# Kernel optimization log

Measured on AMD Instinct MI355X. Metric: run time of the kernel, lower is better.

Reference implementation:

```python
import jax, jax.numpy as jnp
import numpy as np
from jax import lax

SIM_THRESH = 0.9
MOTION_SCALE = 0.5
SALIENCY_SCALE = 0.5
EPS = 1e-6


def setup_inputs() -> dict:
    key = jax.random.key(0)
    k1, k2, k3, k4 = jax.random.split(key, 4)
    B, N, D, H, W = 128, 196, 768, 14, 14
    return {
        "tokens": jax.random.normal(k1, (B, N, D), dtype=jnp.float32),
        "motion_magnitude": jax.random.uniform(k2, (B, 1, H, W), dtype=jnp.float32),
        "saliency_map": jax.random.uniform(k3, (B, 1, H, W), dtype=jnp.float32),
        "compression_ratio": jax.random.uniform(k4, (B, H, W), dtype=jnp.float32),
    }


def _importance(motion, saliency, ratio):
    # motion/saliency are already (B,1,14,14) == (height,width), so
    # adaptive_avg_pool2d to (14,14) is the identity.
    B = motion.shape[0]
    m = motion.reshape(B, -1)
    m = m / (jnp.max(m) + EPS)               # global max, as in torch .max()
    s = saliency.reshape(B, -1)
    s = s / (jnp.max(s) + EPS)
    r = ratio.reshape(B, -1)
    imp = (MOTION_SCALE * m + SALIENCY_SCALE * s
           + (1.0 - MOTION_SCALE - SALIENCY_SCALE) * r)
    lo = imp.min(axis=1, keepdims=True)
    hi = imp.max(axis=1, keepdims=True)
    return (imp - lo) / (hi - lo + EPS)      # (B, N)


def _groups(adj):
    """Sequential BFS grouping over roots, faithful to the torch loop.

    adj: bool (N,N) directed edge mask. Returns (group_ids int32 (N,), num_groups).
    """
    N = adj.shape[0]

    def root_step(carry, r):
        assigned, gids, gid = carry

        def assign(c):
            assigned, gids, gid = c
            # BFS from root r, only through currently-unassigned nodes
            allowed = (~assigned).at[r].set(True)
            reach0 = jnp.zeros(N, dtype=bool).at[r].set(True)

            def body(s):
                reach, _ = s
                nxt = reach | (jnp.any(adj & reach[:, None], axis=0) & allowed)
                return nxt, jnp.any(nxt != reach)

            reach, _ = lax.while_loop(lambda s: s[1], body, (reach0, True))
            return assigned | reach, jnp.where(reach, gid, gids), gid + 1

        carry = lax.cond(assigned[r], lambda c: c, assign, carry)
        return carry, None

    init = (jnp.zeros(N, dtype=bool), jnp.zeros(N, dtype=jnp.int32), jnp.int32(0))
    (_, gids, ngroups), _ = lax.scan(root_step, init, jnp.arange(N))
    return gids, ngroups


def _merge_one(tokens_b, imp_b, adj_b):
    N = tokens_b.shape[0]
    gids, ng = _groups(adj_b)
    denom = jax.ops.segment_sum(imp_b, gids, num_segments=N) + EPS
    w = imp_b / denom[gids]
    merged = jax.ops.segment_sum(tokens_b * w[:, None], gids, num_segments=N)
    return merged, gids, ng


def reference(tokens, motion_magnitude, saliency_map, compression_ratio):
    B, N, D = tokens.shape
    imp = _importance(motion_magnitude, saliency_map, compression_ratio)  # (B,N)

    # cosine similarity (F.normalize with eps=1e-12)
    norm = jnp.maximum(jnp.linalg.norm(tokens, axis=-1, keepdims=True), 1e-12)
    tn = tokens / norm
    sim = jnp.einsum('bnd,bmd->bnm', tn, tn)
    sim = sim * (1.0 - jnp.eye(N, dtype=sim.dtype))  # zero diagonal

    # directed merge mask: similarity * (1 - importance_row)
    mask = (sim > SIM_THRESH).astype(sim.dtype) * (1.0 - imp[:, :, None])
    adj = mask > 0.5

    merged, gids, ng = jax.vmap(_merge_one)(tokens, imp, adj)
    # merged padded to N groups (rows >= num_groups are zero)
    return merged, sim, imp, gids
```

## Files before the change

### kernel.cpp

```cpp
#include <hip/hip_runtime.h>
#include <cstdint>

static constexpr int cB = 128;
static constexpr int cN = 196;
static constexpr int cD = 768;
static constexpr int cNN = cN * cN;
static constexpr int cND = cN * cD;
static constexpr float cEPS = 1e-6f;
static constexpr size_t cBND = (size_t)cB * cN * cD;

typedef __attribute__((ext_vector_type(8))) short short8;
typedef __attribute__((ext_vector_type(4))) float f32x4;
typedef unsigned long long u64;

__device__ __forceinline__ unsigned short bf16_rne(float x) {
    unsigned u = __builtin_bit_cast(unsigned, x);
    u += 0x7FFFu + ((u >> 16) & 1u);
    return (unsigned short)(u >> 16);
}

__global__ __launch_bounds__(256) void k_imp(const float* __restrict__ mo,
                                             const float* __restrict__ sa,
                                             float* __restrict__ out_imp,
                                             float* __restrict__ ws_imp,
                                             float* __restrict__ ws_w,
                                             u64* __restrict__ ws_adj) {
    int b = blockIdx.x, t = threadIdx.x;
    __shared__ float redm[4], reds[4], lo_s[4], hi_s[4], MS[2], LOHI[2];

    for (int i = b * 256 + t; i < cB * cN * 4; i += cB * 256) ws_adj[i] = 0ull;

    float mm = 0.f, ms = 0.f;
    for (int i = t; i < cB * cN; i += 256) {
        mm = fmaxf(mm, mo[i]);
        ms = fmaxf(ms, sa[i]);
    }
    #pragma unroll
    for (int off = 32; off; off >>= 1) {
        mm = fmaxf(mm, __shfl_down(mm, off));
        ms = fmaxf(ms, __shfl_down(ms, off));
    }
    if ((t & 63) == 0) { redm[t >> 6] = mm; reds[t >> 6] = ms; }
    __syncthreads();
    if (t == 0) {
        float a = redm[0], c = reds[0];
        for (int w = 1; w < 4; w++) { a = fmaxf(a, redm[w]); c = fmaxf(c, reds[w]); }
        MS[0] = 1.0f / (a + cEPS);
        MS[1] = 1.0f / (c + cEPS);
    }
    __syncthreads();
    float Minv = MS[0], Sinv = MS[1];
    float v = 0.f, lo = 1e30f, hi = -1e30f;
    if (t < cN) {
        v = 0.5f * mo[b * cN + t] * Minv + 0.5f * sa[b * cN + t] * Sinv;
        lo = v; hi = v;
    }
    #pragma unroll
    for (int off = 32; off; off >>= 1) {
        lo = fminf(lo, __shfl_down(lo, off));
        hi = fmaxf(hi, __shfl_down(hi, off));
    }
    if ((t & 63) == 0) { lo_s[t >> 6] = lo; hi_s[t >> 6] = hi; }
    __syncthreads();
    if (t == 0) {
        float l = lo_s[0], h = hi_s[0];
        for (int w = 1; w < 4; w++) { l = fminf(l, lo_s[w]); h = fmaxf(h, hi_s[w]); }
        LOHI[0] = l; LOHI[1] = h;
    }
    __syncthreads();
    if (t < cN) {
        float imp = (v - LOHI[0]) / (LOHI[1] - LOHI[0] + cEPS);
        out_imp[b * cN + t] = imp;
        ws_imp[b * cN + t] = imp;
        ws_w[b * cN + t] = imp / (imp + cEPS);
    }
}

__global__ __launch_bounds__(256) void k_prep(const float* __restrict__ tok,
                                              const float* __restrict__ ws_w,
                                              unsigned short* __restrict__ plane,
                                              float* __restrict__ ws_invn,
                                              float* __restrict__ merged,
                                              int write_merged) {
    int wid = blockIdx.x * 4 + (threadIdx.x >> 6);
    int lane = threadIdx.x & 63;
    if (wid >= cB * cN) return;
    const float4* p4 = (const float4*)(tok + (size_t)wid * cD);
    float4 v[3];
    float s = 0.f;
    #pragma unroll
    for (int r = 0; r < 3; r++) {
        v[r] = p4[lane + 64 * r];
        s += v[r].x * v[r].x + v[r].y * v[r].y + v[r].z * v[r].z + v[r].w * v[r].w;
    }
    #pragma unroll
    for (int off = 32; off; off >>= 1) s += __shfl_xor(s, off);
    if (lane == 0) ws_invn[wid] = 1.0f / fmaxf(sqrtf(s), 1e-12f);
    float w = ws_w[wid];
    ushort4* hp = (ushort4*)(plane + (size_t)wid * cD);
    float4* mp = (float4*)(merged + (size_t)wid * cD);
    #pragma unroll
    for (int r = 0; r < 3; r++) {
        ushort4 h;
        h.x = bf16_rne(v[r].x);
        h.y = bf16_rne(v[r].y);
        h.z = bf16_rne(v[r].z);
        h.w = bf16_rne(v[r].w);
        hp[lane + 64 * r] = h;
        if (write_merged) {
            float4 m = v[r];
            m.x *= w; m.y *= w; m.z *= w; m.w *= w;
            mp[lane + 64 * r] = m;
        }
    }
}

__global__ __launch_bounds__(256, 2) void k_sim(const unsigned short* __restrict__ plane,
                                                const float* __restrict__ ws_invn,
                                                const float* __restrict__ ws_imp,
                                                float* __restrict__ out_sim,
                                                u64* __restrict__ ws_adj) {
    __shared__ unsigned short sA[128 * 40];
    __shared__ unsigned short sB[128 * 40];
    __shared__ float invR[128], invC[128], impR[128];
    __shared__ u64 ldsAdj[256];

    int bid = blockIdx.x;
    int xcd = bid & 7;
    int lin = bid >> 3;
    int b   = xcd + 8 * (lin >> 2);
    int tile = lin & 3;
    int rb = (tile >> 1) * 128, cb = (tile & 1) * 128;

    int t = threadIdx.x;
    int w = t >> 6, lane = t & 63;
    int lr = lane & 15, kf = (lane >> 4) * 8;
    int wr = (w >> 1) * 64, wc = (w & 1) * 64;

    const size_t bN = (size_t)b * cN;

    ldsAdj[t] = 0ull;
    if (t < 128) {
        int gr = rb + t;
        invR[t] = (gr < cN) ? ws_invn[bN + gr] : 0.f;
        impR[t] = (gr < cN) ? ws_imp[bN + gr] : 1.f;
    } else {
        int gc = cb + (t - 128);
        invC[t - 128] = (gc < cN) ? ws_invn[bN + gc] : 0.f;
    }

    f32x4 acc[4][4];
    #pragma unroll
    for (int i = 0; i < 4; i++)
        #pragma unroll
        for (int j = 0; j < 4; j++) acc[i][j] = (f32x4){0.f, 0.f, 0.f, 0.f};

    int srow = t >> 2;
    int q = t & 3;

    for (int k0 = 0; k0 < cD; k0 += 32) {
        #pragma unroll
        for (int p = 0; p < 2; ++p) {
            int row = srow + 64 * p;
            size_t koff = (size_t)k0 + 8 * q;
            uint4 va = make_uint4(0u, 0u, 0u, 0u), vb = va;
            int gr = rb + row;
            if (gr < cN) va = *(const uint4*)(plane + (bN + gr) * cD + koff);
            int gc = cb + row;
            if (gc < cN) vb = *(const uint4*)(plane + (bN + gc) * cD + koff);
            *(uint4*)&sA[row * 40 + 8 * q] = va;
            *(uint4*)&sB[row * 40 + 8 * q] = vb;
        }
        __syncthreads();

        short8 af[4], bf[4];
        #pragma unroll
        for (int rg = 0; rg < 4; rg++)
            af[rg] = *(const short8*)&sA[(wr + 16 * rg + lr) * 40 + kf];
        #pragma unroll
        for (int cg = 0; cg < 4; cg++)
            bf[cg] = *(const short8*)&sB[(wc + 16 * cg + lr) * 40 + kf];
        #pragma unroll
        for (int rg = 0; rg < 4; rg++)
            #pragma unroll
            for (int cg = 0; cg < 4; cg++)
                acc[rg][cg] = __builtin_amdgcn_mfma_f32_16x16x32_bf16(af[rg], bf[cg], acc[rg][cg], 0, 0, 0);
        __syncthreads();
    }

    float* so = out_sim + (size_t)b * cNN;
    int wloc = w >> 1;
    #pragma unroll
    for (int rg = 0; rg < 4; rg++) {
        int rBaseLoc = wr + 16 * rg + (lane >> 4) * 4;
        #pragma unroll
        for (int cg = 0; cg < 4; cg++) {
            int cLoc = wc + 16 * cg + lr;
            int C = cb + cLoc;
            if (C >= cN) continue;
            float ic = invC[cLoc];
            u64 bits = 0ull;
            #pragma unroll
            for (int i = 0; i < 4; i++) {
                int rLoc = rBaseLoc + i;
                int R = rb + rLoc;
                if (R >= cN) continue;
                float val = (R == C) ? 0.f : acc[rg][cg][i] * invR[rLoc] * ic;
                so[(size_t)R * cN + C] = val;
                if (val > 0.9f && impR[rLoc] < 0.5f) bits |= 1ull << (R & 63);
            }
            if (bits) atomicOr(&ldsAdj[cLoc * 2 + wloc], bits);
        }
    }
    __syncthreads();
    {
        int cLoc = t >> 1, wl = t & 1;
        int C = cb + cLoc;
        u64 v = ldsAdj[t];
        if (C < cN && v)
            atomicOr(&ws_adj[((size_t)b * cN + C) * 4 + (rb >> 6) + wl], v);
    }
}

__global__ __launch_bounds__(256) void k_group(const u64* __restrict__ ws_adj,
                                               const float* __restrict__ ws_imp,
                                               const float* __restrict__ tok,
                                               float* __restrict__ out_gids,
                                               float* __restrict__ ws_w,
                                               int* __restrict__ ws_flag,
                                               int* __restrict__ ws_gids,
                                               float* __restrict__ merged,
                                               int merged_mode) {
    int b = blockIdx.x, t = threadIdx.x;
    __shared__ float impL[cN];
    __shared__ u64 reachw[4], assignedw[4], edge_s[4];
    __shared__ int flag;
    __shared__ int gidsL[cN];
    __shared__ float denomL[cN];
    __shared__ float wL[cN];

    u64 m0 = 0, m1 = 0, m2 = 0, m3 = 0;
    if (t < cN) {
        impL[t] = ws_imp[b * cN + t];
        const u64* ap = ws_adj + ((size_t)b * cN + t) * 4;
        m0 = ap[0]; m1 = ap[1]; m2 = ap[2]; m3 = ap[3];
    }
    u64 anym = m0 | m1 | m2 | m3;
    u64 bal = __ballot(anym != 0ull);
    if ((t & 63) == 0) edge_s[t >> 6] = bal;
    __syncthreads();
    bool has_edges = (edge_s[0] | edge_s[1] | edge_s[2] | edge_s[3]) != 0ull;

    if (!has_edges) {
        if (t < cN) {
            float imp = impL[t];
            ws_w[b * cN + t] = imp / (imp + cEPS);
            ws_gids[b * cN + t] = t;
            out_gids[b * cN + t] = (float)t;
        }
        if (t == 0) ws_flag[b] = 1;
        return;
    }

    if (t < 4) assignedw[t] = 0ull;
    if (t < cN) { gidsL[t] = 0; denomL[t] = 0.f; }
    __syncthreads();
    int gid = 0;
    int wrd_t = t >> 6, bit_t = t & 63;
    for (int r = 0; r < cN; r++) {
        if ((assignedw[r >> 6] >> (r & 63)) & 1ull) continue;
        if (t < 4) reachw[t] = (t == (r >> 6)) ? (1ull << (r & 63)) : 0ull;
        __syncthreads();
        int changed = 1;
        while (changed) {
            u64 hit = (m0 & reachw[0]) | (m1 & reachw[1]) |
                      (m2 & reachw[2]) | (m3 & reachw[3]);
            bool inre = (t < cN) && ((reachw[wrd_t] >> bit_t) & 1ull);
            bool unass = (t < cN) && !((assignedw[wrd_t] >> bit_t) & 1ull);
            bool p = inre || (hit != 0ull && unass);
            u64 nw = __ballot(p);
            __syncthreads();
            if (t == 0) flag = 0;
            __syncthreads();
            if ((t & 63) == 0) {
                if (nw != reachw[t >> 6]) flag = 1;
                reachw[t >> 6] = nw;
            }
            __syncthreads();
            changed = flag;
        }
        if ((t < cN) && ((reachw[wrd_t] >> bit_t) & 1ull)) gidsL[t] = gid;
        if (t < 4) assignedw[t] |= reachw[t];
        gid++;
        __syncthreads();
    }
    if (t < cN) atomicAdd(&denomL[gidsL[t]], impL[t]);
    __syncthreads();
    if (t < cN) {
        int g = gidsL[t];
        float wv = impL[t] / (denomL[g] + cEPS);
        ws_w[b * cN + t] = wv;
        wL[t] = wv;
        ws_gids[b * cN + t] = g;
        out_gids[b * cN + t] = (float)g;
    }
    if (t == 0) ws_flag[b] = 0;
    __syncthreads();

    if (merged_mode == 1) {
        if (t < 192) {
            for (int n = 0; n < cN; n++) {
                float4 acc = make_float4(0.f, 0.f, 0.f, 0.f);
                for (int j = 0; j < cN; j++) {
                    if (gidsL[j] == n) {
                        const float4 v = *(const float4*)(tok + (size_t)b * cND + (size_t)j * cD + 4 * t);
                        float wv = wL[j];
                        acc.x += v.x * wv; acc.y += v.y * wv;
                        acc.z += v.z * wv; acc.w += v.w * wv;
                    }
                }
                *(float4*)(merged + (size_t)b * cND + (size_t)n * cD + 4 * t) = acc;
            }
        }
    }
}

__global__ void k_merge(const float* __restrict__ tok, const float* __restrict__ ws_w,
                        const int* __restrict__ ws_flag, const int* __restrict__ ws_gids,
                        float* __restrict__ out) {
    int b = blockIdx.y;
    int idx4 = blockIdx.x * 256 + threadIdx.x;
    int n = idx4 / 192, d4 = idx4 - n * 192;
    size_t e = (size_t)b * cND + (size_t)n * cD + 4 * d4;
    if (ws_flag[b]) {
        float wv = ws_w[b * cN + n];
        float4 v = *(const float4*)(tok + e);
        v.x *= wv; v.y *= wv; v.z *= wv; v.w *= wv;
        *(float4*)(out + e) = v;
    } else {
        float4 acc = make_float4(0.f, 0.f, 0.f, 0.f);
        const int* g = ws_gids + b * cN;
        const float* wp = ws_w + b * cN;
        const float* tb = tok + (size_t)b * cND + 4 * d4;
        for (int j = 0; j < cN; j++) {
            if (g[j] == n) {
                float4 v = *(const float4*)(tb + (size_t)j * cD);
                float wv = wp[j];
                acc.x += v.x * wv; acc.y += v.y * wv; acc.z += v.z * wv; acc.w += v.w * wv;
            }
        }
        *(float4*)(out + e) = acc;
    }
}

extern "C" void kernel_launch(void* const* d_in, const int* in_sizes, int n_in,
                              void* d_out, int out_size, void* d_ws, size_t ws_size,
                              hipStream_t stream) {
    const float* tok = (const float*)d_in[0];
    const float* mo  = (const float*)d_in[1];
    const float* sa  = (const float*)d_in[2];

    float* out = (float*)d_out;
    float* out_merged = out;
    float* out_sim    = out + cBND;
    float* out_imp    = out_sim + (size_t)cB * cNN;
    float* out_gids   = out_imp + (size_t)cB * cN;

    u64*   ws_adj  = (u64*)d_ws;
    float* ws_imp  = (float*)(ws_adj + (size_t)cB * cN * 4);
    float* ws_w    = ws_imp + cB * cN;
    float* ws_invn = ws_w + cB * cN;
    int*   ws_flag = (int*)(ws_invn + cB * cN);
    int*   ws_gids = ws_flag + cB;

    const size_t plane_off = 2u << 20;
    const size_t need = plane_off + cBND * sizeof(unsigned short);
    const bool pathA = ws_size >= need;

    unsigned short* plane = pathA
        ? (unsigned short*)((char*)d_ws + plane_off)
        : (unsigned short*)out_merged;

    k_imp<<<cB, 256, 0, stream>>>(mo, sa, out_imp, ws_imp, ws_w, ws_adj);
    k_prep<<<(cB * cN + 3) / 4, 256, 0, stream>>>(tok, ws_w, plane, ws_invn,
                                                  out_merged, pathA ? 1 : 0);
    k_sim<<<512, 256, 0, stream>>>(plane, ws_invn, ws_imp, out_sim, ws_adj);
    k_group<<<cB, 256, 0, stream>>>(ws_adj, ws_imp, tok, out_gids, ws_w,
                                    ws_flag, ws_gids, out_merged, pathA ? 1 : 0);
    if (!pathA)
        k_merge<<<dim3(147, cB), 256, 0, stream>>>(tok, ws_w, ws_flag, ws_gids, out_merged);
}
```

Before: 239.3 us.

## Store bf16 plane in MFMA fragment order and load directly to registers

k_prep now writes the bf16 token copy in a pre-swizzled tile layout: 16-row groups by 32-wide k-chunks, arranged so that each lane's MFMA fragment is one contiguous 16-byte load. k_sim drops its LDS staging and per-step barriers, reads fragments straight from global memory, and double-buffers the register loads across k-chunks. Fully out-of-range 16-row groups skip their loads and MFMAs. This removes LDS traffic and synchronisation from the matmul loop, at the cost of repeated global/L2 reads of the same fragments across waves and more register use.

Result: slower. 253.1 us (+5.8%).

```diff
diff --git a/kernel.cpp b/kernel.cpp
--- a/kernel.cpp
+++ b/kernel.cpp
@@ -6,6 +6,9 @@
 static constexpr int cD = 768;
 static constexpr int cNN = cN * cN;
 static constexpr int cND = cN * cD;
+static constexpr int cG  = 13;
+static constexpr int cKC = cD / 32;
+static constexpr int cTILE = 1024;
 static constexpr float cEPS = 1e-6f;
 static constexpr size_t cBND = (size_t)cB * cN * cD;
 
@@ -82,37 +85,40 @@
                                               float* __restrict__ ws_invn,
                                               float* __restrict__ merged,
                                               int write_merged) {
-    int wid = blockIdx.x * 4 + (threadIdx.x >> 6);
-    int lane = threadIdx.x & 63;
-    if (wid >= cB * cN) return;
-    const float4* p4 = (const float4*)(tok + (size_t)wid * cD);
-    float4 v[3];
+    __shared__ unsigned short lp[cKC * 512];
+    int g = blockIdx.x, b = blockIdx.y;
+    int t = threadIdx.x;
+    int lr = t >> 4, q = t & 15;
+    int n = 16 * g + lr;
+    bool valid = n < cN;
+    const size_t row = (size_t)b * cN + (valid ? n : 0);
+    const float4* src = (const float4*)(tok + row * cD);
+    float4* mdst = (float4*)(merged + row * cD);
+    float wv = (valid && write_merged) ? ws_w[row] : 0.f;
     float s = 0.f;
     #pragma unroll
-    for (int r = 0; r < 3; r++) {
-        v[r] = p4[lane + 64 * r];
-        s += v[r].x * v[r].x + v[r].y * v[r].y + v[r].z * v[r].z + v[r].w * v[r].w;
-    }
-    #pragma unroll
-    for (int off = 32; off; off >>= 1) s += __shfl_xor(s, off);
-    if (lane == 0) ws_invn[wid] = 1.0f / fmaxf(sqrtf(s), 1e-12f);
-    float w = ws_w[wid];
-    ushort4* hp = (ushort4*)(plane + (size_t)wid * cD);
-    float4* mp = (float4*)(merged + (size_t)wid * cD);
-    #pragma unroll
-    for (int r = 0; r < 3; r++) {
+    for (int r = 0; r < 12; r++) {
+        float4 v = make_float4(0.f, 0.f, 0.f, 0.f);
+        if (valid) v = src[q + 16 * r];
+        s += v.x * v.x + v.y * v.y + v.z * v.z + v.w * v.w;
+        if (write_merged && valid) {
+            float4 m = make_float4(v.x * wv, v.y * wv, v.z * wv, v.w * wv);
+            mdst[q + 16 * r] = m;
+        }
         ushort4 h;
-        h.x = bf16_rne(v[r].x);
-        h.y = bf16_rne(v[r].y);
-        h.z = bf16_rne(v[r].z);
-        h.w = bf16_rne(v[r].w);
-        hp[lane + 64 * r] = h;
-        if (write_merged) {
-            float4 m = v[r];
-            m.x *= w; m.y *= w; m.z *= w; m.w *= w;
-            mp[lane + 64 * r] = m;
-        }
-    }
+        h.x = bf16_rne(v.x); h.y = bf16_rne(v.y);
+        h.z = bf16_rne(v.z); h.w = bf16_rne(v.w);
+        int off = ((q >> 3) + 2 * r) * 1024 + ((q >> 1) & 3) * 256 + lr * 16 + (q & 1) * 8;
+        *(ushort4*)((char*)lp + off) = h;
+    }
+    #pragma unroll
+    for (int o = 1; o < 16; o <<= 1) s += __shfl_xor(s, o);
+    if (valid && q == 0) ws_invn[row] = 1.0f / fmaxf(sqrtf(s), 1e-12f);
+    __syncthreads();
+    uint4* dst = (uint4*)((char*)plane + ((size_t)b * cG + g) * (cKC * cTILE));
+    const uint4* sl = (const uint4*)lp;
+    #pragma unroll
+    for (int i = 0; i < 6; i++) dst[t + 256 * i] = sl[t + 256 * i];
 }
 
 __global__ __launch_bounds__(256, 2) void k_sim(const unsigned short* __restrict__ plane,
@@ -120,8 +126,6 @@
                                                 const float* __restrict__ ws_imp,
                                                 float* __restrict__ out_sim,
                                                 u64* __restrict__ ws_adj) {
-    __shared__ unsigned short sA[128 * 40];
-    __shared__ unsigned short sB[128 * 40];
     __shared__ float invR[128], invC[128], impR[128];
     __shared__ u64 ldsAdj[256];
 
@@ -134,9 +138,7 @@
 
     int t = threadIdx.x;
     int w = t >> 6, lane = t & 63;
-    int lr = lane & 15, kf = (lane >> 4) * 8;
     int wr = (w >> 1) * 64, wc = (w & 1) * 64;
-
     const size_t bN = (size_t)b * cN;
 
     ldsAdj[t] = 0ull;
@@ -148,6 +150,20 @@
         int gc = cb + (t - 128);
         invC[t - 128] = (gc < cN) ? ws_invn[bN + gc] : 0.f;
     }
+    __syncthreads();
+
+    int rg0 = (rb + wr) >> 4, cg0 = (cb + wc) >> 4;
+    int RG = min(4, cG - rg0), CG = min(4, cG - cg0);
+
+    const char* base = (const char*)plane + (size_t)b * (cG * cKC * cTILE)
+                     + (size_t)lane * 16;
+    const char* pA[4]; const char* pB[4];
+    #pragma unroll
+    for (int rg = 0; rg < 4; rg++)
+        pA[rg] = base + (size_t)min(rg0 + rg, cG - 1) * (cKC * cTILE);
+    #pragma unroll
+    for (int cg = 0; cg < 4; cg++)
+        pB[cg] = base + (size_t)min(cg0 + cg, cG - 1) * (cKC * cTILE);
 
     f32x4 acc[4][4];
     #pragma unroll
@@ -155,37 +171,35 @@
         #pragma unroll
         for (int j = 0; j < 4; j++) acc[i][j] = (f32x4){0.f, 0.f, 0.f, 0.f};
 
-    int srow = t >> 2;
-    int q = t & 3;
-
-    for (int k0 = 0; k0 < cD; k0 += 32) {
-        #pragma unroll
-        for (int p = 0; p < 2; ++p) {
-            int row = srow + 64 * p;
-            size_t koff = (size_t)k0 + 8 * q;
-            uint4 va = make_uint4(0u, 0u, 0u, 0u), vb = va;
-            int gr = rb + row;
-            if (gr < cN) va = *(const uint4*)(plane + (bN + gr) * cD + koff);
-            int gc = cb + row;
-            if (gc < cN) vb = *(const uint4*)(plane + (bN + gc) * cD + koff);
-            *(uint4*)&sA[row * 40 + 8 * q] = va;
-            *(uint4*)&sB[row * 40 + 8 * q] = vb;
-        }
-        __syncthreads();
-
-        short8 af[4], bf[4];
+    short8 A0[4], B0[4], A1[4], B1[4];
+    #pragma unroll
+    for (int i = 0; i < 4; i++) { A0[i] = (short8)0; B0[i] = (short8)0;
+                                  A1[i] = (short8)0; B1[i] = (short8)0; }
+
+    auto LD = [&](short8* Af, short8* Bf, int kc) {
         #pragma unroll
         for (int rg = 0; rg < 4; rg++)
-            af[rg] = *(const short8*)&sA[(wr + 16 * rg + lr) * 40 + kf];
+            if (rg < RG) Af[rg] = *(const short8*)(pA[rg] + (size_t)kc * cTILE);
         #pragma unroll
         for (int cg = 0; cg < 4; cg++)
-            bf[cg] = *(const short8*)&sB[(wc + 16 * cg + lr) * 40 + kf];
+            if (cg < CG) Bf[cg] = *(const short8*)(pB[cg] + (size_t)kc * cTILE);
+    };
+    auto MM = [&](const short8* Af, const short8* Bf) {
         #pragma unroll
         for (int rg = 0; rg < 4; rg++)
             #pragma unroll
             for (int cg = 0; cg < 4; cg++)
-                acc[rg][cg] = __builtin_amdgcn_mfma_f32_16x16x32_bf16(af[rg], bf[cg], acc[rg][cg], 0, 0, 0);
-        __syncthreads();
+                if (rg < RG && cg < CG)
+                    acc[rg][cg] = __builtin_amdgcn_mfma_f32_16x16x32_bf16(
+                        Af[rg], Bf[cg], acc[rg][cg], 0, 0, 0);
+    };
+
+    LD(A0, B0, 0);
+    for (int kc = 0; kc < cKC; kc += 2) {
+        LD(A1, B1, kc + 1);
+        MM(A0, B0);
+        if (kc + 2 < cKC) LD(A0, B0, kc + 2);
+        MM(A1, B1);
     }
 
     float* so = out_sim + (size_t)b * cNN;
@@ -195,7 +209,7 @@
         int rBaseLoc = wr + 16 * rg + (lane >> 4) * 4;
         #pragma unroll
         for (int cg = 0; cg < 4; cg++) {
-            int cLoc = wc + 16 * cg + lr;
+            int cLoc = wc + 16 * cg + (lane & 15);
             int C = cb + cLoc;
             if (C >= cN) continue;
             float ic = invC[cLoc];
@@ -374,7 +388,8 @@
     int*   ws_gids = ws_flag + cB;
 
     const size_t plane_off = 2u << 20;
-    const size_t need = plane_off + cBND * sizeof(unsigned short);
+    const size_t plane_bytes = (size_t)cB * cG * cKC * cTILE;
+    const size_t need = plane_off + plane_bytes;
     const bool pathA = ws_size >= need;
 
     unsigned short* plane = pathA
@@ -382,8 +397,8 @@
         : (unsigned short*)out_merged;
 
     k_imp<<<cB, 256, 0, stream>>>(mo, sa, out_imp, ws_imp, ws_w, ws_adj);
-    k_prep<<<(cB * cN + 3) / 4, 256, 0, stream>>>(tok, ws_w, plane, ws_invn,
-                                                  out_merged, pathA ? 1 : 0);
+    k_prep<<<dim3(cG, cB), 256, 0, stream>>>(tok, ws_w, plane, ws_invn,
+                                             out_merged, pathA ? 1 : 0);
     k_sim<<<512, 256, 0, stream>>>(plane, ws_invn, ws_imp, out_sim, ws_adj);
     k_group<<<cB, 256, 0, stream>>>(ws_adj, ws_imp, tok, out_gids, ws_w,
                                     ws_flag, ws_gids, out_merged, pathA ? 1 : 0);
```

## Convert fp32 tokens to bf16 inside sim GEMM loader, drop bf16 plane

Applied to the files above, without the earlier changes.

The prep kernel no longer writes a separate bf16 copy of the tokens. The similarity GEMM now reads fp32 tokens directly and rounds them to bf16 while staging into shared memory. This removes one full write and re-read of a B*N*D bf16 buffer, but doubles the global bytes each GEMM tile loads. The fallback path (k_merge, workspace-size check) is removed, prep is remapped to half-wave per token, and the importance max reduction is vectorized with float4.

After: 218.8 us. 1.09x faster.

```diff
diff --git a/kernel.cpp b/kernel.cpp
--- a/kernel.cpp
+++ b/kernel.cpp
@@ -10,6 +10,7 @@
 static constexpr size_t cBND = (size_t)cB * cN * cD;
 
 typedef __attribute__((ext_vector_type(8))) short short8;
+typedef __attribute__((ext_vector_type(8))) unsigned short u16x8;
 typedef __attribute__((ext_vector_type(4))) float f32x4;
 typedef unsigned long long u64;
 
@@ -30,10 +31,13 @@
 
     for (int i = b * 256 + t; i < cB * cN * 4; i += cB * 256) ws_adj[i] = 0ull;
 
+    const float4* mo4 = (const float4*)mo;
+    const float4* sa4 = (const float4*)sa;
     float mm = 0.f, ms = 0.f;
-    for (int i = t; i < cB * cN; i += 256) {
-        mm = fmaxf(mm, mo[i]);
-        ms = fmaxf(ms, sa[i]);
+    for (int i = t; i < cB * cN / 4; i += 256) {
+        float4 a = mo4[i], c = sa4[i];
+        mm = fmaxf(mm, fmaxf(fmaxf(a.x, a.y), fmaxf(a.z, a.w)));
+        ms = fmaxf(ms, fmaxf(fmaxf(c.x, c.y), fmaxf(c.z, c.w)));
     }
     #pragma unroll
     for (int off = 32; off; off >>= 1) {
@@ -78,44 +82,31 @@
 
 __global__ __launch_bounds__(256) void k_prep(const float* __restrict__ tok,
                                               const float* __restrict__ ws_w,
-                                              unsigned short* __restrict__ plane,
                                               float* __restrict__ ws_invn,
-                                              float* __restrict__ merged,
-                                              int write_merged) {
-    int wid = blockIdx.x * 4 + (threadIdx.x >> 6);
-    int lane = threadIdx.x & 63;
-    if (wid >= cB * cN) return;
-    const float4* p4 = (const float4*)(tok + (size_t)wid * cD);
-    float4 v[3];
+                                              float* __restrict__ merged) {
+    int t = threadIdx.x;
+    int tk = blockIdx.x * 8 + (t >> 5);
+    int l  = t & 31;
+    const float4* src = (const float4*)(tok + (size_t)tk * cD) + l;
+    float4* dst = (float4*)(merged + (size_t)tk * cD) + l;
+    float w = ws_w[tk];
+    float4 v[6];
+    #pragma unroll
+    for (int j = 0; j < 6; j++) v[j] = src[32 * j];
     float s = 0.f;
     #pragma unroll
-    for (int r = 0; r < 3; r++) {
-        v[r] = p4[lane + 64 * r];
-        s += v[r].x * v[r].x + v[r].y * v[r].y + v[r].z * v[r].z + v[r].w * v[r].w;
-    }
-    #pragma unroll
-    for (int off = 32; off; off >>= 1) s += __shfl_xor(s, off);
-    if (lane == 0) ws_invn[wid] = 1.0f / fmaxf(sqrtf(s), 1e-12f);
-    float w = ws_w[wid];
-    ushort4* hp = (ushort4*)(plane + (size_t)wid * cD);
-    float4* mp = (float4*)(merged + (size_t)wid * cD);
-    #pragma unroll
-    for (int r = 0; r < 3; r++) {
-        ushort4 h;
-        h.x = bf16_rne(v[r].x);
-        h.y = bf16_rne(v[r].y);
-        h.z = bf16_rne(v[r].z);
-        h.w = bf16_rne(v[r].w);
-        hp[lane + 64 * r] = h;
-        if (write_merged) {
-            float4 m = v[r];
-            m.x *= w; m.y *= w; m.z *= w; m.w *= w;
-            mp[lane + 64 * r] = m;
-        }
-    }
-}
-
-__global__ __launch_bounds__(256, 2) void k_sim(const unsigned short* __restrict__ plane,
+    for (int j = 0; j < 6; j++) {
+        float4 x = v[j];
+        s += x.x * x.x + x.y * x.y + x.z * x.z + x.w * x.w;
+        dst[32 * j] = make_float4(x.x * w, x.y * w, x.z * w, x.w * w);
+    }
+    s += __shfl_xor(s, 1);  s += __shfl_xor(s, 2);
+    s += __shfl_xor(s, 4);  s += __shfl_xor(s, 8);
+    s += __shfl_xor(s, 16);
+    if (l == 0) ws_invn[tk] = 1.0f / fmaxf(sqrtf(s), 1e-12f);
+}
+
+__global__ __launch_bounds__(256, 2) void k_sim(const float* __restrict__ tok,
                                                 const float* __restrict__ ws_invn,
                                                 const float* __restrict__ ws_imp,
                                                 float* __restrict__ out_sim,
@@ -136,8 +127,8 @@
     int w = t >> 6, lane = t & 63;
     int lr = lane & 15, kf = (lane >> 4) * 8;
     int wr = (w >> 1) * 64, wc = (w & 1) * 64;
-
     const size_t bN = (size_t)b * cN;
+    const float* tb = tok + bN * cD;
 
     ldsAdj[t] = 0ull;
     if (t < 128) {
@@ -162,14 +153,30 @@
         #pragma unroll
         for (int p = 0; p < 2; ++p) {
             int row = srow + 64 * p;
-            size_t koff = (size_t)k0 + 8 * q;
-            uint4 va = make_uint4(0u, 0u, 0u, 0u), vb = va;
+            int koff = k0 + 8 * q;
+            float4 a0 = make_float4(0.f, 0.f, 0.f, 0.f), a1 = a0;
+            float4 b0 = a0, b1 = a0;
             int gr = rb + row;
-            if (gr < cN) va = *(const uint4*)(plane + (bN + gr) * cD + koff);
+            if (gr < cN) {
+                const float4* pa = (const float4*)(tb + (size_t)gr * cD + koff);
+                a0 = pa[0]; a1 = pa[1];
+            }
             int gc = cb + row;
-            if (gc < cN) vb = *(const uint4*)(plane + (bN + gc) * cD + koff);
-            *(uint4*)&sA[row * 40 + 8 * q] = va;
-            *(uint4*)&sB[row * 40 + 8 * q] = vb;
+            if (gc < cN) {
+                const float4* pb = (const float4*)(tb + (size_t)gc * cD + koff);
+                b0 = pb[0]; b1 = pb[1];
+            }
+            u16x8 ha, hb;
+            ha[0] = bf16_rne(a0.x); ha[1] = bf16_rne(a0.y);
+            ha[2] = bf16_rne(a0.z); ha[3] = bf16_rne(a0.w);
+            ha[4] = bf16_rne(a1.x); ha[5] = bf16_rne(a1.y);
+            ha[6] = bf16_rne(a1.z); ha[7] = bf16_rne(a1.w);
+            hb[0] = bf16_rne(b0.x); hb[1] = bf16_rne(b0.y);
+            hb[2] = bf16_rne(b0.z); hb[3] = bf16_rne(b0.w);
+            hb[4] = bf16_rne(b1.x); hb[5] = bf16_rne(b1.y);
+            hb[6] = bf16_rne(b1.z); hb[7] = bf16_rne(b1.w);
+            *(u16x8*)&sA[row * 40 + 8 * q] = ha;
+            *(u16x8*)&sB[row * 40 + 8 * q] = hb;
         }
         __syncthreads();
 
@@ -229,8 +236,7 @@
                                                float* __restrict__ ws_w,
                                                int* __restrict__ ws_flag,
                                                int* __restrict__ ws_gids,
-                                               float* __restrict__ merged,
-                                               int merged_mode) {
+                                               float* __restrict__ merged) {
     int b = blockIdx.x, t = threadIdx.x;
     __shared__ float impL[cN];
     __shared__ u64 reachw[4], assignedw[4], edge_s[4];
@@ -307,49 +313,19 @@
     if (t == 0) ws_flag[b] = 0;
     __syncthreads();
 
-    if (merged_mode == 1) {
-        if (t < 192) {
-            for (int n = 0; n < cN; n++) {
-                float4 acc = make_float4(0.f, 0.f, 0.f, 0.f);
-                for (int j = 0; j < cN; j++) {
-                    if (gidsL[j] == n) {
-                        const float4 v = *(const float4*)(tok + (size_t)b * cND + (size_t)j * cD + 4 * t);
-                        float wv = wL[j];
-                        acc.x += v.x * wv; acc.y += v.y * wv;
-                        acc.z += v.z * wv; acc.w += v.w * wv;
-                    }
+    if (t < 192) {
+        for (int n = 0; n < cN; n++) {
+            float4 acc = make_float4(0.f, 0.f, 0.f, 0.f);
+            for (int j = 0; j < cN; j++) {
+                if (gidsL[j] == n) {
+                    const float4 v = *(const float4*)(tok + (size_t)b * cND + (size_t)j * cD + 4 * t);
+                    float wv = wL[j];
+                    acc.x += v.x * wv; acc.y += v.y * wv;
+                    acc.z += v.z * wv; acc.w += v.w * wv;
                 }
-                *(float4*)(merged + (size_t)b * cND + (size_t)n * cD + 4 * t) = acc;
-            }
-        }
-    }
-}
-
-__global__ void k_merge(const float* __restrict__ tok, const float* __restrict__ ws_w,
-                        const int* __restrict__ ws_flag, const int* __restrict__ ws_gids,
-                        float* __restrict__ out) {
-    int b = blockIdx.y;
-    int idx4 = blockIdx.x * 256 + threadIdx.x;
-    int n = idx4 / 192, d4 = idx4 - n * 192;
-    size_t e = (size_t)b * cND + (size_t)n * cD + 4 * d4;
-    if (ws_flag[b]) {
-        float wv = ws_w[b * cN + n];
-        float4 v = *(const float4*)(tok + e);
-        v.x *= wv; v.y *= wv; v.z *= wv; v.w *= wv;
-        *(float4*)(out + e) = v;
-    } else {
-        float4 acc = make_float4(0.f, 0.f, 0.f, 0.f);
-        const int* g = ws_gids + b * cN;
-        const float* wp = ws_w + b * cN;
-        const float* tb = tok + (size_t)b * cND + 4 * d4;
-        for (int j = 0; j < cN; j++) {
-            if (g[j] == n) {
-                float4 v = *(const float4*)(tb + (size_t)j * cD);
-                float wv = wp[j];
-                acc.x += v.x * wv; acc.y += v.y * wv; acc.z += v.z * wv; acc.w += v.w * wv;
-            }
-        }
-        *(float4*)(out + e) = acc;
+            }
+            *(float4*)(merged + (size_t)b * cND + (size_t)n * cD + 4 * t) = acc;
+        }
     }
 }
 
@@ -373,20 +349,9 @@
     int*   ws_flag = (int*)(ws_invn + cB * cN);
     int*   ws_gids = ws_flag + cB;
 
-    const size_t plane_off = 2u << 20;
-    const size_t need = plane_off + cBND * sizeof(unsigned short);
-    const bool pathA = ws_size >= need;
-
-    unsigned short* plane = pathA
-        ? (unsigned short*)((char*)d_ws + plane_off)
-        : (unsigned short*)out_merged;
-
     k_imp<<<cB, 256, 0, stream>>>(mo, sa, out_imp, ws_imp, ws_w, ws_adj);
-    k_prep<<<(cB * cN + 3) / 4, 256, 0, stream>>>(tok, ws_w, plane, ws_invn,
-                                                  out_merged, pathA ? 1 : 0);
-    k_sim<<<512, 256, 0, stream>>>(plane, ws_invn, ws_imp, out_sim, ws_adj);
+    k_prep<<<cB * cN / 8, 256, 0, stream>>>(tok, ws_w, ws_invn, out_merged);
+    k_sim<<<512, 256, 0, stream>>>(tok, ws_invn, ws_imp, out_sim, ws_adj);
     k_group<<<cB, 256, 0, stream>>>(ws_adj, ws_imp, tok, out_gids, ws_w,
-                                    ws_flag, ws_gids, out_merged, pathA ? 1 : 0);
-    if (!pathA)
-        k_merge<<<dim3(147, cB), 256, 0, stream>>>(tok, ws_w, ws_flag, ws_gids, out_merged);
-}
+                                    ws_flag, ws_gids, out_merged);
+}
```
